# Performance work log

Hardware: AMD Instinct MI355X
Metric: run time of the kernel (lower is better)

The kernel has to match this reference:

```python
import jax, jax.numpy as jnp
import numpy as np

DIV_COEF = 1.0
EPS = 1e-8  # torch.cosine_similarity default eps


def setup_inputs() -> dict:
    key = jax.random.key(0)
    id_ = jax.random.normal(key, (8192, 512), dtype=jnp.float32)
    return {"id": id_}


def reference(id):
    # cosine similarity via norm + GEMM (math identical to broadcast form)
    norms = jnp.linalg.norm(id, axis=1)                      # [N]
    dots = id @ id.T                                          # [N, N]
    sim = dots / jnp.maximum(norms[:, None] * norms[None, :], EPS)
    n = id.shape[0]
    # zero diagonal, clamp negatives to zero, mean over full NxN
    off_diag = 1.0 - jnp.eye(n, dtype=sim.dtype)
    id_sim = off_diag * sim
    l_id_div = jnp.mean(jnp.where(id_sim < 0, 0.0, id_sim))
    total_loss = DIV_COEF * l_id_div
    return (total_loss, l_id_div)
```

## Files before the change

kernel.cpp:

```cpp
#include <hip/hip_runtime.h>
#include <stdint.h>

#define NROWS 8192
#define KDIM  512
#define BM    128
#define BK    128
#define NKI   (KDIM / BK)
#define NT    (NROWS / BM)
#define NBLK  (NT * (NT + 1) / 2)

typedef __attribute__((ext_vector_type(4)))  int   i32x4;
typedef __attribute__((ext_vector_type(8)))  int   i32x8;
typedef __attribute__((ext_vector_type(16))) float f32x16;

__device__ __forceinline__ void async_copy16(const unsigned char* g, unsigned char* l) {
  __builtin_amdgcn_global_load_lds(
      (const __attribute__((address_space(1))) unsigned int*)g,
      (__attribute__((address_space(3))) unsigned int*)l,
      16, 0, 0);
}

__global__ __launch_bounds__(256) void prep_kernel(
    const float* __restrict__ src, unsigned char* __restrict__ dst,
    float* __restrict__ acc) {
  const int row  = blockIdx.x * 4 + (threadIdx.x >> 6);
  const int lane = threadIdx.x & 63;
  const float4 v0 = ((const float4*)src)[row * 128 + lane * 2];
  const float4 v1 = ((const float4*)src)[row * 128 + lane * 2 + 1];
  float ss = v0.x * v0.x + v0.y * v0.y + v0.z * v0.z + v0.w * v0.w
           + v1.x * v1.x + v1.y * v1.y + v1.z * v1.z + v1.w * v1.w;
  #pragma unroll
  for (int off = 32; off > 0; off >>= 1) ss += __shfl_down(ss, off);
  const float rn = 1.0f / sqrtf(__shfl(ss, 0));
  if (row == 0 && lane == 0) *acc = 0.0f;
  int pk0 = __builtin_amdgcn_cvt_pk_fp8_f32(v0.x * rn, v0.y * rn, 0, false);
  pk0     = __builtin_amdgcn_cvt_pk_fp8_f32(v0.z * rn, v0.w * rn, pk0, true);
  int pk1 = __builtin_amdgcn_cvt_pk_fp8_f32(v1.x * rn, v1.y * rn, 0, false);
  pk1     = __builtin_amdgcn_cvt_pk_fp8_f32(v1.z * rn, v1.w * rn, pk1, true);
  const int cg  = lane >> 1;
  const int win = cg >> 3;
  const int p   = (cg & 7) ^ (row & 7);
  const int hf  = lane & 1;
  uint2 o; o.x = (unsigned int)pk0; o.y = (unsigned int)pk1;
  ((uint2*)dst)[row * 64 + win * 16 + p * 2 + hf] = o;
}

__device__ __forceinline__ int tri_base(int b) {
  return b * NT - (b * (b - 1)) / 2;
}

__global__ __launch_bounds__(256) void sim_reduce_kernel(
    const unsigned char* __restrict__ idn, float* __restrict__ acc) {
  const int idx = blockIdx.x;
  const float Af = 2.0f * NT + 1.0f;
  int bi = (int)((Af - sqrtf(Af * Af - 8.0f * (float)idx)) * 0.5f);
  while (bi > 0 && tri_base(bi) > idx) bi--;
  while (tri_base(bi + 1) <= idx) bi++;
  const int bj = bi + (idx - tri_base(bi));

  __shared__ __align__(16) unsigned char As[2][BM * BK];
  __shared__ __align__(16) unsigned char Bs[2][BM * BK];

  const int tid  = threadIdx.x;
  const int lane = tid & 63;
  const int w    = tid >> 6;
  const int wr   = (w >> 1) * 64;
  const int wc   = (w & 1) * 64;
  const int r32  = lane & 31;
  const int h    = lane >> 5;
  const int rx   = r32 & 7;

  f32x16 acc_f[2][2];
  #pragma unroll
  for (int i = 0; i < 2; i++)
    #pragma unroll
    for (int j = 0; j < 2; j++)
      acc_f[i][j] = (f32x16){0.f, 0.f, 0.f, 0.f, 0.f, 0.f, 0.f, 0.f,
                             0.f, 0.f, 0.f, 0.f, 0.f, 0.f, 0.f, 0.f};

  const unsigned char* gA = idn + (size_t)(bi * BM + (tid >> 3)) * KDIM + (tid & 7) * 16;
  const unsigned char* gB = idn + (size_t)(bj * BM + (tid >> 3)) * KDIM + (tid & 7) * 16;
  const int ldso = tid * 16;

  #pragma unroll
  for (int i = 0; i < 4; i++) async_copy16(gA + (size_t)i * 16384, &As[0][ldso + i * 4096]);
  #pragma unroll
  for (int i = 0; i < 4; i++) async_copy16(gB + (size_t)i * 16384, &Bs[0][ldso + i * 4096]);

  #pragma unroll
  for (int t = 0; t < NKI; ++t) {
    const int cs = t & 1;
    if (t + 1 < NKI) {
      const int ns = cs ^ 1;
      const int ko = (t + 1) * BK;
      #pragma unroll
      for (int i = 0; i < 4; i++)
        async_copy16(gA + ko + (size_t)i * 16384, &As[ns][ldso + i * 4096]);
      #pragma unroll
      for (int i = 0; i < 4; i++)
        async_copy16(gB + ko + (size_t)i * 16384, &Bs[ns][ldso + i * 4096]);
      asm volatile("s_waitcnt vmcnt(8)" ::: "memory");
    } else {
      asm volatile("s_waitcnt vmcnt(0)" ::: "memory");
    }
    asm volatile("s_barrier" ::: "memory");

    #pragma unroll
    for (int ks = 0; ks < 2; ks++) {
      const int c0 = 4 * ks + 2 * h;
      const int p0 = ((c0)     ^ rx) * 16;
      const int p1 = ((c0 + 1) ^ rx) * 16;
      i32x8 af[2], bf[2];
      #pragma unroll
      for (int mi = 0; mi < 2; mi++) {
        const unsigned char* ab = &As[cs][(wr + mi * 32 + r32) * BK];
        const i32x4 alo = *(const i32x4*)(ab + p0);
        const i32x4 ahi = *(const i32x4*)(ab + p1);
        af[mi] = __builtin_shufflevector(alo, ahi, 0, 1, 2, 3, 4, 5, 6, 7);
        const unsigned char* bb = &Bs[cs][(wc + mi * 32 + r32) * BK];
        const i32x4 blo = *(const i32x4*)(bb + p0);
        const i32x4 bhi = *(const i32x4*)(bb + p1);
        bf[mi] = __builtin_shufflevector(blo, bhi, 0, 1, 2, 3, 4, 5, 6, 7);
      }
      #pragma unroll
      for (int mi = 0; mi < 2; mi++)
        #pragma unroll
        for (int ni = 0; ni < 2; ni++)
          acc_f[mi][ni] = __builtin_amdgcn_mfma_scale_f32_32x32x64_f8f6f4(
              af[mi], bf[ni], acc_f[mi][ni],
              0, 0,
              0, 0x7F7F7F7Fu,
              0, 0x7F7F7F7Fu);
    }

    asm volatile("s_barrier" ::: "memory");
  }

  float local = 0.f;
  const bool diag = (bi == bj);
  #pragma unroll
  for (int mi = 0; mi < 2; mi++)
    #pragma unroll
    for (int ni = 0; ni < 2; ni++)
      #pragma unroll
      for (int rg = 0; rg < 16; rg++) {
        const int ri = wr + mi * 32 + (rg & 3) + 8 * (rg >> 2) + 4 * h;
        const int ci = wc + ni * 32 + r32;
        float v = fmaxf(acc_f[mi][ni][rg], 0.f);
        if (diag && ri == ci) v = 0.f;
        local += v;
      }

  #pragma unroll
  for (int off = 32; off > 0; off >>= 1) local += __shfl_down(local, off);
  __syncthreads();
  float* red = (float*)As;
  if (lane == 0) red[w] = local;
  __syncthreads();
  if (tid == 0) {
    float s = red[0] + red[1] + red[2] + red[3];
    if (!diag) s *= 2.f;
    atomicAdd(acc, s);
  }
}

__global__ void finalize_kernel(const float* __restrict__ acc, float* __restrict__ out) {
  const float m = *acc * (1.0f / ((float)NROWS * (float)NROWS));
  out[0] = m;
  out[1] = m;
}

extern "C" void kernel_launch(void* const* d_in, const int* in_sizes, int n_in,
                              void* d_out, int out_size, void* d_ws, size_t ws_size,
                              hipStream_t stream) {
  const float* id = (const float*)d_in[0];
  float* out = (float*)d_out;
  unsigned char* idn = (unsigned char*)d_ws;
  float* acc = (float*)((char*)d_ws + (size_t)NROWS * KDIM);

  prep_kernel<<<NROWS / 4, 256, 0, stream>>>(id, idn, acc);
  sim_reduce_kernel<<<NBLK, 256, 0, stream>>>(idn, acc);
  finalize_kernel<<<1, 1, 0, stream>>>(acc, out);
}
```

Before: 100.8 us.

## Use 256x256 tiles with 8 waves and fold finalize into last-block reduction

```diff
diff --git a/kernel.cpp b/kernel.cpp
--- a/kernel.cpp
+++ b/kernel.cpp
@@ -3,8 +3,8 @@
 
 #define NROWS 8192
 #define KDIM  512
-#define BM    128
-#define BK    128
+#define BM    256
+#define BK    64
 #define NKI   (KDIM / BK)
 #define NT    (NROWS / BM)
 #define NBLK  (NT * (NT + 1) / 2)
@@ -32,25 +32,26 @@
   #pragma unroll
   for (int off = 32; off > 0; off >>= 1) ss += __shfl_down(ss, off);
   const float rn = 1.0f / sqrtf(__shfl(ss, 0));
-  if (row == 0 && lane == 0) *acc = 0.0f;
+  if (row == 0 && lane == 0) { acc[0] = 0.0f; ((unsigned int*)acc)[1] = 0u; }
   int pk0 = __builtin_amdgcn_cvt_pk_fp8_f32(v0.x * rn, v0.y * rn, 0, false);
   pk0     = __builtin_amdgcn_cvt_pk_fp8_f32(v0.z * rn, v0.w * rn, pk0, true);
   int pk1 = __builtin_amdgcn_cvt_pk_fp8_f32(v1.x * rn, v1.y * rn, 0, false);
   pk1     = __builtin_amdgcn_cvt_pk_fp8_f32(v1.z * rn, v1.w * rn, pk1, true);
   const int cg  = lane >> 1;
-  const int win = cg >> 3;
-  const int p   = (cg & 7) ^ (row & 7);
+  const int win = cg >> 2;
+  const int p   = (cg & 3) ^ ((row >> 1) & 3);
   const int hf  = lane & 1;
   uint2 o; o.x = (unsigned int)pk0; o.y = (unsigned int)pk1;
-  ((uint2*)dst)[row * 64 + win * 16 + p * 2 + hf] = o;
+  ((uint2*)dst)[row * 64 + win * 8 + p * 2 + hf] = o;
 }
 
 __device__ __forceinline__ int tri_base(int b) {
   return b * NT - (b * (b - 1)) / 2;
 }
 
-__global__ __launch_bounds__(256) void sim_reduce_kernel(
-    const unsigned char* __restrict__ idn, float* __restrict__ acc) {
+__global__ __launch_bounds__(512, 2) void sim_reduce_kernel(
+    const unsigned char* __restrict__ idn, float* __restrict__ acc,
+    float* __restrict__ out) {
   const int idx = blockIdx.x;
   const float Af = 2.0f * NT + 1.0f;
   int bi = (int)((Af - sqrtf(Af * Af - 8.0f * (float)idx)) * 0.5f);
@@ -64,28 +65,31 @@
   const int tid  = threadIdx.x;
   const int lane = tid & 63;
   const int w    = tid >> 6;
-  const int wr   = (w >> 1) * 64;
-  const int wc   = (w & 1) * 64;
+  const int wrow = (w >> 2) * 128;
+  const int wcol = (w & 3) * 64;
   const int r32  = lane & 31;
   const int h    = lane >> 5;
-  const int rx   = r32 & 7;
+  const int rx   = (r32 >> 1) & 3;
 
-  f32x16 acc_f[2][2];
+  f32x16 acc_f[4][2];
   #pragma unroll
-  for (int i = 0; i < 2; i++)
+  for (int i = 0; i < 4; i++)
     #pragma unroll
     for (int j = 0; j < 2; j++)
       acc_f[i][j] = (f32x16){0.f, 0.f, 0.f, 0.f, 0.f, 0.f, 0.f, 0.f,
                              0.f, 0.f, 0.f, 0.f, 0.f, 0.f, 0.f, 0.f};
 
-  const unsigned char* gA = idn + (size_t)(bi * BM + (tid >> 3)) * KDIM + (tid & 7) * 16;
-  const unsigned char* gB = idn + (size_t)(bj * BM + (tid >> 3)) * KDIM + (tid & 7) * 16;
+  const unsigned char* gA = idn + (size_t)(bi * BM + (tid >> 2)) * KDIM + (tid & 3) * 16;
+  const unsigned char* gB = idn + (size_t)(bj * BM + (tid >> 2)) * KDIM + (tid & 3) * 16;
   const int ldso = tid * 16;
 
   #pragma unroll
-  for (int i = 0; i < 4; i++) async_copy16(gA + (size_t)i * 16384, &As[0][ldso + i * 4096]);
+  for (int i = 0; i < 2; i++) async_copy16(gA + (size_t)i * 65536, &As[0][ldso + i * 8192]);
   #pragma unroll
-  for (int i = 0; i < 4; i++) async_copy16(gB + (size_t)i * 16384, &Bs[0][ldso + i * 4096]);
+  for (int i = 0; i < 2; i++) async_copy16(gB + (size_t)i * 65536, &Bs[0][ldso + i * 8192]);
+
+  const int p0 = ((2 * h)     ^ rx) * 16;
+  const int p1 = ((2 * h + 1) ^ rx) * 16;
 
   #pragma unroll
   for (int t = 0; t < NKI; ++t) {
@@ -94,44 +98,41 @@
       const int ns = cs ^ 1;
       const int ko = (t + 1) * BK;
       #pragma unroll
-      for (int i = 0; i < 4; i++)
-        async_copy16(gA + ko + (size_t)i * 16384, &As[ns][ldso + i * 4096]);
+      for (int i = 0; i < 2; i++)
+        async_copy16(gA + ko + (size_t)i * 65536, &As[ns][ldso + i * 8192]);
       #pragma unroll
-      for (int i = 0; i < 4; i++)
-        async_copy16(gB + ko + (size_t)i * 16384, &Bs[ns][ldso + i * 4096]);
-      asm volatile("s_waitcnt vmcnt(8)" ::: "memory");
+      for (int i = 0; i < 2; i++)
+        async_copy16(gB + ko + (size_t)i * 65536, &Bs[ns][ldso + i * 8192]);
+      asm volatile("s_waitcnt vmcnt(4)" ::: "memory");
     } else {
       asm volatile("s_waitcnt vmcnt(0)" ::: "memory");
     }
     asm volatile("s_barrier" ::: "memory");
 
+    i32x8 af[4], bf[2];
     #pragma unroll
-    for (int ks = 0; ks < 2; ks++) {
-      const int c0 = 4 * ks + 2 * h;
-      const int p0 = ((c0)     ^ rx) * 16;
-      const int p1 = ((c0 + 1) ^ rx) * 16;
-      i32x8 af[2], bf[2];
+    for (int mi = 0; mi < 4; mi++) {
+      const unsigned char* ab = &As[cs][(wrow + mi * 32 + r32) * BK];
+      const i32x4 alo = *(const i32x4*)(ab + p0);
+      const i32x4 ahi = *(const i32x4*)(ab + p1);
+      af[mi] = __builtin_shufflevector(alo, ahi, 0, 1, 2, 3, 4, 5, 6, 7);
+    }
+    #pragma unroll
+    for (int ni = 0; ni < 2; ni++) {
+      const unsigned char* bb = &Bs[cs][(wcol + ni * 32 + r32) * BK];
+      const i32x4 blo = *(const i32x4*)(bb + p0);
+      const i32x4 bhi = *(const i32x4*)(bb + p1);
+      bf[ni] = __builtin_shufflevector(blo, bhi, 0, 1, 2, 3, 4, 5, 6, 7);
+    }
+    #pragma unroll
+    for (int mi = 0; mi < 4; mi++)
       #pragma unroll
-      for (int mi = 0; mi < 2; mi++) {
-        const unsigned char* ab = &As[cs][(wr + mi * 32 + r32) * BK];
-        const i32x4 alo = *(const i32x4*)(ab + p0);
-        const i32x4 ahi = *(const i32x4*)(ab + p1);
-        af[mi] = __builtin_shufflevector(alo, ahi, 0, 1, 2, 3, 4, 5, 6, 7);
-        const unsigned char* bb = &Bs[cs][(wc + mi * 32 + r32) * BK];
-        const i32x4 blo = *(const i32x4*)(bb + p0);
-        const i32x4 bhi = *(const i32x4*)(bb + p1);
-        bf[mi] = __builtin_shufflevector(blo, bhi, 0, 1, 2, 3, 4, 5, 6, 7);
-      }
-      #pragma unroll
-      for (int mi = 0; mi < 2; mi++)
-        #pragma unroll
-        for (int ni = 0; ni < 2; ni++)
-          acc_f[mi][ni] = __builtin_amdgcn_mfma_scale_f32_32x32x64_f8f6f4(
-              af[mi], bf[ni], acc_f[mi][ni],
-              0, 0,
-              0, 0x7F7F7F7Fu,
-              0, 0x7F7F7F7Fu);
-    }
+      for (int ni = 0; ni < 2; ni++)
+        acc_f[mi][ni] = __builtin_amdgcn_mfma_scale_f32_32x32x64_f8f6f4(
+            af[mi], bf[ni], acc_f[mi][ni],
+            0, 0,
+            0, 0x7F7F7F7Fu,
+            0, 0x7F7F7F7Fu);
 
     asm volatile("s_barrier" ::: "memory");
   }
@@ -139,13 +140,13 @@
   float local = 0.f;
   const bool diag = (bi == bj);
   #pragma unroll
-  for (int mi = 0; mi < 2; mi++)
+  for (int mi = 0; mi < 4; mi++)
     #pragma unroll
     for (int ni = 0; ni < 2; ni++)
       #pragma unroll
       for (int rg = 0; rg < 16; rg++) {
-        const int ri = wr + mi * 32 + (rg & 3) + 8 * (rg >> 2) + 4 * h;
-        const int ci = wc + ni * 32 + r32;
+        const int ri = wrow + mi * 32 + (rg & 3) + 8 * (rg >> 2) + 4 * h;
+        const int ci = wcol + ni * 32 + r32;
         float v = fmaxf(acc_f[mi][ni][rg], 0.f);
         if (diag && ri == ci) v = 0.f;
         local += v;
@@ -158,16 +159,19 @@
   if (lane == 0) red[w] = local;
   __syncthreads();
   if (tid == 0) {
-    float s = red[0] + red[1] + red[2] + red[3];
+    float s = red[0] + red[1] + red[2] + red[3]
+            + red[4] + red[5] + red[6] + red[7];
     if (!diag) s *= 2.f;
     atomicAdd(acc, s);
+    __threadfence();
+    unsigned int done = atomicAdd((unsigned int*)(acc + 1), 1u);
+    if (done == NBLK - 1) {
+      float total = atomicAdd(acc, 0.0f);
+      const float m = total * (1.0f / ((float)NROWS * (float)NROWS));
+      out[0] = m;
+      out[1] = m;
+    }
   }
-}
-
-__global__ void finalize_kernel(const float* __restrict__ acc, float* __restrict__ out) {
-  const float m = *acc * (1.0f / ((float)NROWS * (float)NROWS));
-  out[0] = m;
-  out[1] = m;
 }
 
 extern "C" void kernel_launch(void* const* d_in, const int* in_sizes, int n_in,
@@ -179,6 +183,5 @@
   float* acc = (float*)((char*)d_ws + (size_t)NROWS * KDIM);
 
   prep_kernel<<<NROWS / 4, 256, 0, stream>>>(id, idn, acc);
-  sim_reduce_kernel<<<NBLK, 256, 0, stream>>>(idn, acc);
-  finalize_kernel<<<1, 1, 0, stream>>>(acc, out);
+  sim_reduce_kernel<<<NBLK, 512, 0, stream>>>(idn, acc, out);
 }
```

Result: faster. 96.34 us (-4.4%).
